# Performance work log

Measured on AMD Instinct MI355X. Metric: run time of the kernel, lower is better.

Reference implementation:

```python
import jax, jax.numpy as jnp
import numpy as np

N_HEAD = 16


def setup_inputs() -> dict:
    B, T, C, H = 64, 128, 2048, N_HEAD
    hd = C // H
    key = jax.random.key(0)
    ks = jax.random.split(key, 5)
    x = jax.random.normal(ks[0], (B, T, C), dtype=jnp.float32)
    wq = jax.random.normal(ks[1], (C, C), dtype=jnp.float32) * 0.02
    wk = jax.random.normal(ks[2], (C, C), dtype=jnp.float32) * 0.02
    wv = jax.random.normal(ks[3], (C, C), dtype=jnp.float32) * 0.02
    wo = jax.random.normal(ks[4], (C, C), dtype=jnp.float32) * 0.02
    # RoPE frequencies: freqs_cis = exp(i * pos * theta_j), theta_j = 10000^(-2j/hd)
    pos = jnp.arange(T, dtype=jnp.float32)
    inv_freq = 1.0 / (10000.0 ** (jnp.arange(0, hd, 2, dtype=jnp.float32) / hd))  # [hd/2]
    ang = pos[:, None] * inv_freq[None, :]  # [T, hd/2]
    return {
        "x": x,
        "freqs_cos": jnp.cos(ang),
        "freqs_sin": jnp.sin(ang),
        "wq": wq, "wk": wk, "wv": wv, "wo": wo,
    }


def _apply_rope(t, cos, sin):
    # t: [B,T,H,hd]; complex multiply on interleaved (even, odd) pairs
    B, T, H, hd = t.shape
    tr = t.reshape(B, T, H, hd // 2, 2)
    te, to = tr[..., 0], tr[..., 1]
    c = cos[None, :, None, :]  # [1,T,1,hd/2]
    s = sin[None, :, None, :]
    oe = te * c - to * s
    oo = te * s + to * c
    return jnp.stack([oe, oo], axis=-1).reshape(B, T, H, hd)


def reference(x, freqs_cos, freqs_sin, wq, wk, wv, wo):
    B, T, C = x.shape
    H = N_HEAD
    hd = C // H
    q = (x @ wq.T).reshape(B, T, H, hd)
    k = (x @ wk.T).reshape(B, T, H, hd)
    v = (x @ wv.T).reshape(B, T, H, hd)
    q = _apply_rope(q, freqs_cos, freqs_sin)
    k = _apply_rope(k, freqs_cos, freqs_sin)
    # scores: [B,H,T,S]
    scores = jnp.einsum("bthd,bshd->bhts", q, k) / (hd ** 0.5)
    causal = jnp.tril(jnp.ones((T, T), dtype=bool))
    scores = jnp.where(causal[None, None], scores, jnp.float32(-jnp.inf))
    probs = jax.nn.softmax(scores, axis=-1)  # dropout is identity in eval
    out = jnp.einsum("bhts,bshd->bthd", probs, v).reshape(B, T, C)
    return out @ wo.T
```

## Files before the change

kernel.cpp:

```cpp
#include <hip/hip_runtime.h>
#include <cstdint>


typedef unsigned short ushort;
typedef __bf16 bf16x8 __attribute__((ext_vector_type(8)));
typedef float floatx4 __attribute__((ext_vector_type(4)));

__device__ __forceinline__ ushort f2bf(float f) {
  union { float f; uint32_t u; } v; v.f = f;
  uint32_t r = v.u + 0x7FFFu + ((v.u >> 16) & 1u);
  return (ushort)(r >> 16);
}
__device__ __forceinline__ float bf2f(ushort h) {
  union { uint32_t u; float f; } v; v.u = ((uint32_t)h) << 16;
  return v.f;
}

__device__ __forceinline__ void load_lds16(const void* g, void* l) {
  __builtin_amdgcn_global_load_lds(
      (__attribute__((address_space(1))) void*)(uintptr_t)g,
      (__attribute__((address_space(3))) void*)(uint32_t)(uintptr_t)l,
      16, 0, 0);
}

__device__ __forceinline__ void store_out(ushort* C, size_t i, float v) { C[i] = f2bf(v); }
__device__ __forceinline__ void store_out(float* C, size_t i, float v) { C[i] = v; }

template <typename OutT>
__device__ __forceinline__ void gemm_bt_body(const ushort* __restrict__ A,
                                             const ushort* __restrict__ B,
                                             OutT* __restrict__ C,
                                             int M, int N, int K) {
  __shared__ __align__(16) ushort As[128 * 32];
  __shared__ __align__(16) ushort Bs[128 * 32];
  const int tid = threadIdx.x;
  const int wave = tid >> 6, lane = tid & 63;
  const int quad = lane >> 4, colv = lane & 15;
  const int m0 = blockIdx.x * 128, n0 = blockIdx.y * 128;
  const int wm = (wave & 1) * 64, wn = (wave >> 1) * 64;

  floatx4 acc[4][4] = {};

  const int e0 = tid * 8;
  const int row0 = e0 >> 5;
  const int c0 = e0 & 31;

  for (int k0 = 0; k0 < K; k0 += 32) {
    if (k0) __syncthreads();
    const ushort* Ab = A + (size_t)(m0 + row0) * K + k0 + c0;
    const ushort* Bb = B + (size_t)(n0 + row0) * K + k0 + c0;
    load_lds16(Ab, &As[wave * 512]);
    load_lds16(Bb, &Bs[wave * 512]);
    load_lds16(Ab + (size_t)64 * K, &As[wave * 512 + 2048]);
    load_lds16(Bb + (size_t)64 * K, &Bs[wave * 512 + 2048]);
    __syncthreads();

    bf16x8 af[4], bfr[4];
#pragma unroll
    for (int i = 0; i < 4; ++i)
      af[i] = *(const bf16x8*)&As[(wm + i * 16 + colv) * 32 + quad * 8];
#pragma unroll
    for (int j = 0; j < 4; ++j)
      bfr[j] = *(const bf16x8*)&Bs[(wn + j * 16 + colv) * 32 + quad * 8];
#pragma unroll
    for (int i = 0; i < 4; ++i)
#pragma unroll
      for (int j = 0; j < 4; ++j)
        acc[i][j] = __builtin_amdgcn_mfma_f32_16x16x32_bf16(af[i], bfr[j], acc[i][j], 0, 0, 0);
  }

#pragma unroll
  for (int i = 0; i < 4; ++i)
#pragma unroll
    for (int j = 0; j < 4; ++j)
#pragma unroll
      for (int r = 0; r < 4; ++r) {
        int m = m0 + wm + i * 16 + quad * 4 + r;
        int n = n0 + wn + j * 16 + colv;
        store_out(C, (size_t)m * N + n, acc[i][j][r]);
      }
}

__global__ __launch_bounds__(256) void gemm_qkv(
    const ushort* __restrict__ A, const ushort* __restrict__ Wq,
    const ushort* __restrict__ Wk, const ushort* __restrict__ Wv,
    ushort* __restrict__ Q, ushort* __restrict__ Kb, ushort* __restrict__ V) {
  const ushort* B = (blockIdx.z == 0) ? Wq : (blockIdx.z == 1) ? Wk : Wv;
  ushort* C = (blockIdx.z == 0) ? Q : (blockIdx.z == 1) ? Kb : V;
  gemm_bt_body<ushort>(A, B, C, 8192, 2048, 2048);
}

__global__ __launch_bounds__(256) void gemm_out_k(
    const ushort* __restrict__ A, const ushort* __restrict__ B,
    float* __restrict__ C) {
  gemm_bt_body<float>(A, B, C, 8192, 2048, 2048);
}

__global__ void cvt_kernel(const float* __restrict__ in, ushort* __restrict__ out, int n4) {
  int i = blockIdx.x * blockDim.x + threadIdx.x;
  if (i >= n4) return;
  float4 v = ((const float4*)in)[i];
  ushort4 o;
  o.x = f2bf(v.x); o.y = f2bf(v.y); o.z = f2bf(v.z); o.w = f2bf(v.w);
  ((ushort4*)out)[i] = o;
}

__global__ void rope_kernel(ushort* __restrict__ Q, ushort* __restrict__ K,
                            const float* __restrict__ Cf, const float* __restrict__ Sf,
                            int npairs) {
  int idx = blockIdx.x * blockDim.x + threadIdx.x;
  if (idx >= npairs) return;
  int e = idx << 1;
  int i = (e >> 1) & 63;
  int t = (e >> 11) & 127;
  float c = Cf[t * 64 + i], s = Sf[t * 64 + i];
  uint32_t qp = *(uint32_t*)&Q[e];
  float qe = bf2f((ushort)(qp & 0xFFFF)), qo = bf2f((ushort)(qp >> 16));
  *(uint32_t*)&Q[e] = (uint32_t)f2bf(qe * c - qo * s) | ((uint32_t)f2bf(qe * s + qo * c) << 16);
  uint32_t kp = *(uint32_t*)&K[e];
  float ke = bf2f((ushort)(kp & 0xFFFF)), ko = bf2f((ushort)(kp >> 16));
  *(uint32_t*)&K[e] = (uint32_t)f2bf(ke * c - ko * s) | ((uint32_t)f2bf(ke * s + ko * c) << 16);
}

__global__ __launch_bounds__(256) void attn_kernel(
    const ushort* __restrict__ Q, const ushort* __restrict__ K,
    const ushort* __restrict__ V, ushort* __restrict__ O) {
  __shared__ __align__(16) ushort Qs[128 * 128];
  __shared__ __align__(16) ushort KVs[128 * 128];
  const int b = blockIdx.x >> 4, h = blockIdx.x & 15;
  const int tid = threadIdx.x, wave = tid >> 6, lane = tid & 63;
  const int quad = lane >> 4, colv = lane & 15;
  const size_t gbase = (size_t)b * 262144 + (size_t)h * 128;

#pragma unroll
  for (int sgi = 0; sgi < 8; ++sgi) {
    int seg = tid + sgi * 256;
    int t = seg >> 4, g = seg & 15;
    uint4 qv = *(const uint4*)(Q + gbase + (size_t)t * 2048 + g * 8);
    uint4 kv = *(const uint4*)(K + gbase + (size_t)t * 2048 + g * 8);
    int so = t * 128 + ((g ^ (t & 15)) << 3);
    *(uint4*)&Qs[so] = qv;
    *(uint4*)&KVs[so] = kv;
  }
  __syncthreads();

  floatx4 accs[2][8] = {};
#pragma unroll
  for (int kc = 0; kc < 4; ++kc) {
    bf16x8 af[2], bfr[8];
#pragma unroll
    for (int i = 0; i < 2; ++i) {
      int r = wave * 32 + i * 16 + colv;
      af[i] = *(const bf16x8*)&Qs[r * 128 + ((((kc << 2) | quad) ^ (r & 15)) << 3)];
    }
#pragma unroll
    for (int j = 0; j < 8; ++j) {
      int r = j * 16 + colv;
      bfr[j] = *(const bf16x8*)&KVs[r * 128 + ((((kc << 2) | quad) ^ (r & 15)) << 3)];
    }
#pragma unroll
    for (int i = 0; i < 2; ++i)
#pragma unroll
      for (int j = 0; j < 8; ++j)
        accs[i][j] = __builtin_amdgcn_mfma_f32_16x16x32_bf16(af[i], bfr[j], accs[i][j], 0, 0, 0);
  }

  const float scale = 0.08838834764831845f;
#pragma unroll
  for (int i = 0; i < 2; ++i)
#pragma unroll
    for (int r = 0; r < 4; ++r) {
      int t = wave * 32 + i * 16 + quad * 4 + r;
      float mx = -1e30f;
#pragma unroll
      for (int j = 0; j < 8; ++j) {
        int s = j * 16 + colv;
        float v = accs[i][j][r] * scale;
        v = (s <= t) ? v : -1e30f;
        accs[i][j][r] = v;
        mx = fmaxf(mx, v);
      }
#pragma unroll
      for (int off = 1; off < 16; off <<= 1) mx = fmaxf(mx, __shfl_xor(mx, off, 64));
      float l = 0.f;
#pragma unroll
      for (int j = 0; j < 8; ++j) {
        float p = __expf(accs[i][j][r] - mx);
        accs[i][j][r] = p;
        l += p;
      }
#pragma unroll
      for (int off = 1; off < 16; off <<= 1) l += __shfl_xor(l, off, 64);
      float inv = 1.0f / l;
#pragma unroll
      for (int j = 0; j < 8; ++j) {
        int s = j * 16 + colv;
        Qs[t * 128 + ((((s >> 3) ^ (t & 15)) << 3) | (s & 7))] = f2bf(accs[i][j][r] * inv);
      }
    }
  __syncthreads();

#pragma unroll
  for (int sgi = 0; sgi < 8; ++sgi) {
    int seg = tid + sgi * 256;
    int t = seg >> 4;
    int dg = (seg & 15) << 3;
    uint4 vv = *(const uint4*)(V + gbase + (size_t)t * 2048 + dg);
    const ushort* vp = (const ushort*)&vv;
#pragma unroll
    for (int jj = 0; jj < 8; ++jj) {
      int d = dg + jj;
      KVs[d * 128 + ((((t >> 3) ^ (d & 15)) << 3) | (t & 7))] = vp[jj];
    }
  }
  __syncthreads();

  floatx4 acco[2][8] = {};
#pragma unroll
  for (int kc = 0; kc < 4; ++kc) {
    bf16x8 af[2], bfr[8];
#pragma unroll
    for (int i = 0; i < 2; ++i) {
      int r = wave * 32 + i * 16 + colv;
      af[i] = *(const bf16x8*)&Qs[r * 128 + ((((kc << 2) | quad) ^ (r & 15)) << 3)];
    }
#pragma unroll
    for (int j = 0; j < 8; ++j) {
      int r = j * 16 + colv;
      bfr[j] = *(const bf16x8*)&KVs[r * 128 + ((((kc << 2) | quad) ^ (r & 15)) << 3)];
    }
#pragma unroll
    for (int i = 0; i < 2; ++i)
#pragma unroll
      for (int j = 0; j < 8; ++j)
        acco[i][j] = __builtin_amdgcn_mfma_f32_16x16x32_bf16(af[i], bfr[j], acco[i][j], 0, 0, 0);
  }

#pragma unroll
  for (int i = 0; i < 2; ++i)
#pragma unroll
    for (int j = 0; j < 8; ++j)
#pragma unroll
      for (int r = 0; r < 4; ++r) {
        int t = wave * 32 + i * 16 + quad * 4 + r;
        int d = j * 16 + colv;
        O[gbase + (size_t)t * 2048 + d] = f2bf(acco[i][j][r]);
      }
}

extern "C" void kernel_launch(void* const* d_in, const int* in_sizes, int n_in,
                              void* d_out, int out_size, void* d_ws, size_t ws_size,
                              hipStream_t stream) {
  const float* x    = (const float*)d_in[0];
  const float* fcos = (const float*)d_in[1];
  const float* fsin = (const float*)d_in[2];
  const float* wq   = (const float*)d_in[3];
  const float* wk   = (const float*)d_in[4];
  const float* wv   = (const float*)d_in[5];
  const float* wo   = (const float*)d_in[6];
  float* out = (float*)d_out;

  const size_t CC = 2048ull * 2048ull;
  const size_t MC = 8192ull * 2048ull;
  ushort* wob = (ushort*)d_ws;
  ushort* xb  = wob + CC;
  ushort* wqb = xb + MC;
  ushort* wkb = wqb + CC;
  ushort* wvb = wkb + CC;
  ushort* Qb  = wvb + CC;
  ushort* Kb  = Qb + MC;
  ushort* Vb  = Kb + MC;

  cvt_kernel<<<dim3((unsigned)(MC / 4 / 256)), 256, 0, stream>>>(x, xb, (int)(MC / 4));
  cvt_kernel<<<dim3((unsigned)(CC / 4 / 256)), 256, 0, stream>>>(wq, wqb, (int)(CC / 4));
  cvt_kernel<<<dim3((unsigned)(CC / 4 / 256)), 256, 0, stream>>>(wk, wkb, (int)(CC / 4));
  cvt_kernel<<<dim3((unsigned)(CC / 4 / 256)), 256, 0, stream>>>(wv, wvb, (int)(CC / 4));
  cvt_kernel<<<dim3((unsigned)(CC / 4 / 256)), 256, 0, stream>>>(wo, wob, (int)(CC / 4));

  gemm_qkv<<<dim3(64, 16, 3), 256, 0, stream>>>(xb, wqb, wkb, wvb, Qb, Kb, Vb);
  rope_kernel<<<dim3((unsigned)(MC / 2 / 256)), 256, 0, stream>>>(Qb, Kb, fcos, fsin, (int)(MC / 2));
  attn_kernel<<<dim3(1024), 256, 0, stream>>>(Qb, Kb, Vb, xb );
  gemm_out_k<<<dim3(64, 16), 256, 0, stream>>>(xb, wob, out);
}
```

Before: 550.6 us.

## Fuse RoPE into attention Q/K load and merge conversion kernels

Removes the standalone RoPE kernel and applies the rotation while the attention kernel loads Q and K tiles into shared memory, so the extra read and write pass over Q and K in global memory goes away. The five fp32-to-bf16 conversion launches are merged into one kernel that picks its source and destination by index range, which cuts launch overhead. The attention prologue gains extra loads of the cos/sin tables and extra ALU work.

```diff
diff --git a/kernel.cpp b/kernel.cpp
--- a/kernel.cpp
+++ b/kernel.cpp
@@ -96,35 +96,37 @@
   gemm_bt_body<float>(A, B, C, 8192, 2048, 2048);
 }
 
-__global__ void cvt_kernel(const float* __restrict__ in, ushort* __restrict__ out, int n4) {
-  int i = blockIdx.x * blockDim.x + threadIdx.x;
-  if (i >= n4) return;
-  float4 v = ((const float4*)in)[i];
+#define NX 4194304u
+#define NW 1048576u
+__global__ void cvt_all(const float* __restrict__ x, const float* __restrict__ wq,
+                        const float* __restrict__ wk, const float* __restrict__ wv,
+                        const float* __restrict__ wo,
+                        ushort* __restrict__ xb, ushort* __restrict__ wqb,
+                        ushort* __restrict__ wkb, ushort* __restrict__ wvb,
+                        ushort* __restrict__ wob) {
+  uint32_t i = blockIdx.x * 256u + threadIdx.x;
+  const float* src;
+  ushort* dst;
+  uint32_t off;
+  if (i < NX) {
+    src = x; dst = xb; off = i;
+  } else {
+    uint32_t i2 = i - NX;
+    uint32_t r = i2 >> 20;
+    off = i2 & (NW - 1u);
+    src = (r == 0) ? wq : (r == 1) ? wk : (r == 2) ? wv : wo;
+    dst = (r == 0) ? wqb : (r == 1) ? wkb : (r == 2) ? wvb : wob;
+  }
+  float4 v = ((const float4*)src)[off];
   ushort4 o;
   o.x = f2bf(v.x); o.y = f2bf(v.y); o.z = f2bf(v.z); o.w = f2bf(v.w);
-  ((ushort4*)out)[i] = o;
-}
-
-__global__ void rope_kernel(ushort* __restrict__ Q, ushort* __restrict__ K,
-                            const float* __restrict__ Cf, const float* __restrict__ Sf,
-                            int npairs) {
-  int idx = blockIdx.x * blockDim.x + threadIdx.x;
-  if (idx >= npairs) return;
-  int e = idx << 1;
-  int i = (e >> 1) & 63;
-  int t = (e >> 11) & 127;
-  float c = Cf[t * 64 + i], s = Sf[t * 64 + i];
-  uint32_t qp = *(uint32_t*)&Q[e];
-  float qe = bf2f((ushort)(qp & 0xFFFF)), qo = bf2f((ushort)(qp >> 16));
-  *(uint32_t*)&Q[e] = (uint32_t)f2bf(qe * c - qo * s) | ((uint32_t)f2bf(qe * s + qo * c) << 16);
-  uint32_t kp = *(uint32_t*)&K[e];
-  float ke = bf2f((ushort)(kp & 0xFFFF)), ko = bf2f((ushort)(kp >> 16));
-  *(uint32_t*)&K[e] = (uint32_t)f2bf(ke * c - ko * s) | ((uint32_t)f2bf(ke * s + ko * c) << 16);
+  ((ushort4*)dst)[off] = o;
 }
 
 __global__ __launch_bounds__(256) void attn_kernel(
     const ushort* __restrict__ Q, const ushort* __restrict__ K,
-    const ushort* __restrict__ V, ushort* __restrict__ O) {
+    const ushort* __restrict__ V, const float* __restrict__ Cf,
+    const float* __restrict__ Sf, ushort* __restrict__ O) {
   __shared__ __align__(16) ushort Qs[128 * 128];
   __shared__ __align__(16) ushort KVs[128 * 128];
   const int b = blockIdx.x >> 4, h = blockIdx.x & 15;
@@ -138,6 +140,20 @@
     int t = seg >> 4, g = seg & 15;
     uint4 qv = *(const uint4*)(Q + gbase + (size_t)t * 2048 + g * 8);
     uint4 kv = *(const uint4*)(K + gbase + (size_t)t * 2048 + g * 8);
+    float4 cf = *(const float4*)(Cf + t * 64 + g * 4);
+    float4 sf = *(const float4*)(Sf + t * 64 + g * 4);
+    uint32_t* qw = (uint32_t*)&qv;
+    uint32_t* kw = (uint32_t*)&kv;
+#pragma unroll
+    for (int j = 0; j < 4; ++j) {
+      float c = (&cf.x)[j], s = (&sf.x)[j];
+      uint32_t w = qw[j];
+      float e = bf2f((ushort)(w & 0xFFFF)), o = bf2f((ushort)(w >> 16));
+      qw[j] = (uint32_t)f2bf(e * c - o * s) | ((uint32_t)f2bf(e * s + o * c) << 16);
+      w = kw[j];
+      e = bf2f((ushort)(w & 0xFFFF)); o = bf2f((ushort)(w >> 16));
+      kw[j] = (uint32_t)f2bf(e * c - o * s) | ((uint32_t)f2bf(e * s + o * c) << 16);
+    }
     int so = t * 128 + ((g ^ (t & 15)) << 3);
     *(uint4*)&Qs[so] = qv;
     *(uint4*)&KVs[so] = kv;
@@ -271,14 +287,10 @@
   ushort* Kb  = Qb + MC;
   ushort* Vb  = Kb + MC;
 
-  cvt_kernel<<<dim3((unsigned)(MC / 4 / 256)), 256, 0, stream>>>(x, xb, (int)(MC / 4));
-  cvt_kernel<<<dim3((unsigned)(CC / 4 / 256)), 256, 0, stream>>>(wq, wqb, (int)(CC / 4));
-  cvt_kernel<<<dim3((unsigned)(CC / 4 / 256)), 256, 0, stream>>>(wk, wkb, (int)(CC / 4));
-  cvt_kernel<<<dim3((unsigned)(CC / 4 / 256)), 256, 0, stream>>>(wv, wvb, (int)(CC / 4));
-  cvt_kernel<<<dim3((unsigned)(CC / 4 / 256)), 256, 0, stream>>>(wo, wob, (int)(CC / 4));
+  unsigned cvt_blocks = (unsigned)((MC + 4 * CC) / 4 / 256);
+  cvt_all<<<dim3(cvt_blocks), 256, 0, stream>>>(x, wq, wk, wv, wo, xb, wqb, wkb, wvb, wob);
 
   gemm_qkv<<<dim3(64, 16, 3), 256, 0, stream>>>(xb, wqb, wkb, wvb, Qb, Kb, Vb);
-  rope_kernel<<<dim3((unsigned)(MC / 2 / 256)), 256, 0, stream>>>(Qb, Kb, fcos, fsin, (int)(MC / 2));
-  attn_kernel<<<dim3(1024), 256, 0, stream>>>(Qb, Kb, Vb, xb );
+  attn_kernel<<<dim3(1024), 256, 0, stream>>>(Qb, Kb, Vb, fcos, fsin, xb );
   gemm_out_k<<<dim3(64, 16), 256, 0, stream>>>(xb, wob, out);
 }
```

Measured after the change: 526.7 us. 4.3% less time.
